# Kernel optimization log

Hardware: AMD Instinct MI355X
Metric: run time of the kernel (lower is better)

## Reference

```python
import jax, jax.numpy as jnp
import numpy as np

BATCH, PATH_DIM = 2048, 2048
SIG_DIM = 14  # 2 + 2^2 + 2^3, depth-3 signature of a 2-channel path


def setup_inputs() -> dict:
    key = jax.random.key(0)
    ks = jax.random.split(key, 6)
    x = jax.random.normal(ks[0], (BATCH, 1, PATH_DIM), jnp.float32)
    w1 = jax.random.normal(ks[1], (8, 1), jnp.float32) * 0.5   # Augment conv1 (kernel=1)
    b1 = jax.random.normal(ks[2], (8,), jnp.float32) * 0.1
    w2 = jax.random.normal(ks[3], (2, 8), jnp.float32) * 0.3   # Augment conv2 (kernel=1)
    b2 = jax.random.normal(ks[4], (2,), jnp.float32) * 0.1
    w_out = jax.random.normal(ks[5], (SIG_DIM,), jnp.float32) * 0.2  # Linear(14,1,bias=False)
    return dict(x=x, w1=w1, b1=b1, w2=w2, b2=b2, w_out=w_out)


def _forward(x, w1, b1, w2, b2, w_out):
    # Augment: pointwise MLP (Conv1d, kernel_size=1), channels 1 -> 8 -> 2, ReLU between.
    h = jax.nn.relu(jnp.einsum('bcl,hc->bhl', x, w1) + b1[None, :, None])
    path = jnp.einsum('bhl,oh->bol', h, w2) + b2[None, :, None]   # (B, 2, L)
    p = jnp.transpose(path, (0, 2, 1))                            # (B, L, 2)
    dx = p[:, 1:, :] - p[:, :-1, :]                               # (B, N=L-1, 2) increments

    # Depth-3 signature of each linear segment with increment v:
    #   level1 = v, level2 = v^{\otimes 2}/2, level3 = v^{\otimes 3}/6.
    s1 = dx
    s2 = 0.5 * jnp.einsum('bni,bnj->bnij', dx, dx)
    s3 = (1.0 / 6.0) * jnp.einsum('bni,bnj,bnk->bnijk', dx, dx, dx)

    def chen(carry, seg):
        # Chen's identity: signature of concatenated path = carry \otimes seg.
        a1, a2, a3 = carry
        g1, g2, g3 = seg
        c1 = a1 + g1
        c2 = a2 + jnp.einsum('bi,bj->bij', a1, g1) + g2
        c3 = (a3 + jnp.einsum('bij,bk->bijk', a2, g1)
              + jnp.einsum('bi,bjk->bijk', a1, g2) + g3)
        B = c1.shape[0]
        flat = jnp.concatenate([c1, c2.reshape(B, 4), c3.reshape(B, 8)], axis=-1)  # (B, 14)
        return (c1, c2, c3), flat

    B = dx.shape[0]
    dt = dx.dtype
    init = (jnp.zeros((B, 2), dt), jnp.zeros((B, 2, 2), dt), jnp.zeros((B, 2, 2, 2), dt))
    segs = (jnp.swapaxes(s1, 0, 1), jnp.swapaxes(s2, 0, 1), jnp.swapaxes(s3, 0, 1))
    _, sigs = jax.lax.scan(chen, init, segs)          # (N, B, 14): sig of each prefix x[:,:,:i+2]
    # Tiny output projection Linear(14 -> 1, no bias), then stack/transpose -> (B, N)
    return jnp.einsum('nbs,s->bn', sigs, w_out)


def reference(x, w1, b1, w2, b2, w_out):
    return _forward(x, w1, b1, w2, b2, w_out)
```

## Files before the change

### kernel.cpp

```cpp
#include <hip/hip_runtime.h>

#define LPTS  2048
#define NSEG  2047
#define TPB   256
#define STEPS 8
#define NBATCH 2048
#define NWAVE (TPB / 64)

template <int CTRL, int RMASK, bool BC>
__device__ __forceinline__ float dpp_f(float s) {
    return __int_as_float(__builtin_amdgcn_update_dpp(
        0, __float_as_int(s), CTRL, RMASK, 0xF, BC));
}


__device__ __forceinline__ void chen_step7(float s[7], float vx, float vy,
                                           const float WO[14], float WO78,
                                           float WO1112) {
    const float qxx = 0.5f * vx * vx;
    const float qxy = 0.5f * vx * vy;
    const float qyy = 0.5f * vy * vy;
    const float wx = fmaf(vx, (1.0f / 3.0f), s[0]);
    const float wy = fmaf(vy, (1.0f / 3.0f), s[1]);
    const float tvxx = fmaf(WO[7], vy, WO[6] * vx);
    const float tvxy = fmaf(WO[9], vy, WO[8] * vx);
    const float tvyx = fmaf(WO[11], vy, WO[10] * vx);
    const float tvyy = fmaf(WO[13], vy, WO[12] * vx);
    const float tqx = fmaf(WO[9], qyy, fmaf(WO78, qxy, WO[6] * qxx));
    const float tqy = fmaf(WO[13], qyy, fmaf(WO1112, qxy, WO[10] * qxx));
    float z1 = fmaf(s[2], tvxx, s[6]);
    z1 = fmaf(s[4], tvyx, z1);
    z1 = fmaf(wx, tqx, z1);
    float z2 = fmaf(s[5], tvyy, s[3] * tvxy);
    z2 = fmaf(wy, tqy, z2);
    s[6] = z1 + z2;
    const float ux = fmaf(vx, 0.5f, s[0]);
    const float uy = fmaf(vy, 0.5f, s[1]);
    s[2] = fmaf(ux, vx, s[2]);
    s[3] = fmaf(ux, vy, s[3]);
    s[4] = fmaf(uy, vx, s[4]);
    s[5] = fmaf(uy, vy, s[5]);
    s[0] += vx;
    s[1] += vy;
}

__device__ __forceinline__ void chen_combine7(const float a[7], float b[7],
                                              const float WO[14]) {
    const float tvxx = fmaf(WO[7], b[1], WO[6] * b[0]);
    const float tvxy = fmaf(WO[9], b[1], WO[8] * b[0]);
    const float tvyx = fmaf(WO[11], b[1], WO[10] * b[0]);
    const float tvyy = fmaf(WO[13], b[1], WO[12] * b[0]);
    const float ubx = fmaf(WO[9], b[5], fmaf(WO[8], b[4], fmaf(WO[7], b[3], WO[6] * b[2])));
    const float uby = fmaf(WO[13], b[5], fmaf(WO[12], b[4], fmaf(WO[11], b[3], WO[10] * b[2])));
    float z1 = fmaf(a[2], tvxx, a[6] + b[6]);
    z1 = fmaf(a[4], tvyx, z1);
    z1 = fmaf(a[0], ubx, z1);
    float z2 = fmaf(a[5], tvyy, a[3] * tvxy);
    z2 = fmaf(a[1], uby, z2);
    const float cxx = a[2] + fmaf(a[0], b[0], b[2]);
    const float cxy = a[3] + fmaf(a[0], b[1], b[3]);
    const float cyx = a[4] + fmaf(a[1], b[0], b[4]);
    const float cyy = a[5] + fmaf(a[1], b[1], b[5]);
    b[0] = a[0] + b[0];
    b[1] = a[1] + b[1];
    b[2] = cxx;
    b[3] = cxy;
    b[4] = cyx;
    b[5] = cyy;
    b[6] = z1 + z2;
}

__device__ __forceinline__ void augment(float x,
                                        const float W1[8], const float B1[8],
                                        const float W2x[8], const float W2y[8],
                                        float B2x, float B2y,
                                        float& px, float& py) {
    float ox = B2x, oy = B2y;
#pragma unroll
    for (int c = 0; c < 8; ++c) {
        float h = fmaxf(fmaf(W1[c], x, B1[c]), 0.0f);
        ox = fmaf(W2x[c], h, ox);
        oy = fmaf(W2y[c], h, oy);
    }
    px = ox;
    py = oy;
}

#define SCAN_ROUND(CTRL, RMASK, BC)                                     \
    {                                                                   \
        float p[7];                                                     \
        _Pragma("unroll")                                               \
        for (int i = 0; i < 7; ++i) p[i] = dpp_f<CTRL, RMASK, BC>(s[i]); \
        chen_combine7(p, s, WO);                                        \
    }

__global__ void sig_scan_kernel(
    const float* __restrict__ x, const float* __restrict__ w1,
    const float* __restrict__ b1, const float* __restrict__ w2,
    const float* __restrict__ b2, const float* __restrict__ wout,
    float* __restrict__ out) {
    __shared__ float wsum[NWAVE][8];

    const int t = threadIdx.x;
    const int lane = t & 63;
    const int wv = t >> 6;
    const int brow = blockIdx.x;
    const float* __restrict__ xrow = x + (size_t)brow * LPTS;

    float W1[8], B1[8], W2x[8], W2y[8];
#pragma unroll
    for (int c = 0; c < 8; ++c) {
        W1[c] = w1[c];
        B1[c] = b1[c];
        W2x[c] = w2[c];
        W2y[c] = w2[8 + c];
    }
    const float B2x = b2[0], B2y = b2[1];
    float WO[14];
#pragma unroll
    for (int i = 0; i < 14; ++i) WO[i] = wout[i];
    const float WO78 = WO[7] + WO[8];
    const float WO1112 = WO[11] + WO[12];

    const int n0 = t * STEPS;
    const float4 xa = *reinterpret_cast<const float4*>(xrow + n0);
    const float4 xb = *reinterpret_cast<const float4*>(xrow + n0 + 4);
    const int ib = (n0 + STEPS > LPTS - 1) ? (LPTS - 1) : (n0 + STEPS);
    const float x8 = xrow[ib];
    const float xv[STEPS + 1] = {xa.x, xa.y, xa.z, xa.w,
                                 xb.x, xb.y, xb.z, xb.w, x8};

    float vx[STEPS], vy[STEPS];
    float s[7] = {0, 0, 0, 0, 0, 0, 0};
    float ppx, ppy;
    augment(xv[0], W1, B1, W2x, W2y, B2x, B2y, ppx, ppy);
#pragma unroll
    for (int k = 0; k < STEPS; ++k) {
        float px, py;
        augment(xv[k + 1], W1, B1, W2x, W2y, B2x, B2y, px, py);
        vx[k] = px - ppx;
        vy[k] = py - ppy;
        ppx = px;
        ppy = py;
        chen_step7(s, vx[k], vy[k], WO, WO78, WO1112);
    }

    SCAN_ROUND(0x111, 0xF, true)
    SCAN_ROUND(0x112, 0xF, true)
    SCAN_ROUND(0x114, 0xF, true)
    SCAN_ROUND(0x118, 0xF, true)
    SCAN_ROUND(0x142, 0xA, false)
    SCAN_ROUND(0x143, 0xC, false)

    if (lane == 63) {
#pragma unroll
        for (int i = 0; i < 7; ++i) wsum[wv][i] = s[i];
    }
    __syncthreads();

    float a[7];
#pragma unroll
    for (int i = 0; i < 7; ++i) a[i] = dpp_f<0x138, 0xF, true>(s[i]);
    for (int w = wv - 1; w >= 0; --w) {
        float tw[7];
#pragma unroll
        for (int i = 0; i < 7; ++i) tw[i] = wsum[w][i];
        chen_combine7(tw, a, WO);
    }

    float* __restrict__ orow = out + (size_t)brow * NSEG;
#pragma unroll
    for (int k = 0; k < STEPS; ++k) {
        chen_step7(a, vx[k], vy[k], WO, WO78, WO1112);
        float o = a[6];
        o = fmaf(WO[0], a[0], o);
        o = fmaf(WO[1], a[1], o);
        o = fmaf(WO[2], a[2], o);
        o = fmaf(WO[3], a[3], o);
        o = fmaf(WO[4], a[4], o);
        o = fmaf(WO[5], a[5], o);
        const int n = n0 + k;
        if (n < NSEG) orow[n] = o;
    }
}

extern "C" void kernel_launch(void* const* d_in, const int* in_sizes, int n_in,
                              void* d_out, int out_size, void* d_ws, size_t ws_size,
                              hipStream_t stream) {
    const float* x  = (const float*)d_in[0];
    const float* w1 = (const float*)d_in[1];
    const float* b1 = (const float*)d_in[2];
    const float* w2 = (const float*)d_in[3];
    const float* b2 = (const float*)d_in[4];
    const float* wo = (const float*)d_in[5];
    float* out = (float*)d_out;
    sig_scan_kernel<<<NBATCH, TPB, 0, stream>>>(x, w1, b1, w2, b2, wo, out);
}
```

Before: 21.43 us.

## Process two rows per block and split per-thread chains into parallel halves

```diff
diff --git a/kernel.cpp b/kernel.cpp
--- a/kernel.cpp
+++ b/kernel.cpp
@@ -5,6 +5,8 @@
 #define TPB   256
 #define STEPS 8
 #define NBATCH 2048
+#define ROWS  2
+#define GRIDN (NBATCH / ROWS)
 #define NWAVE (TPB / 64)
 
 template <int CTRL, int RMASK, bool BC>
@@ -86,26 +88,24 @@
     py = oy;
 }
 
-#define SCAN_ROUND(CTRL, RMASK, BC)                                     \
-    {                                                                   \
-        float p[7];                                                     \
-        _Pragma("unroll")                                               \
+#define SCAN_ROUND(CTRL, RMASK, BC)                                      \
+    {                                                                    \
+        float p[7];                                                      \
+        _Pragma("unroll")                                                \
         for (int i = 0; i < 7; ++i) p[i] = dpp_f<CTRL, RMASK, BC>(s[i]); \
-        chen_combine7(p, s, WO);                                        \
-    }
-
-__global__ void sig_scan_kernel(
+        chen_combine7(p, s, WO);                                         \
+    }
+
+__global__ __launch_bounds__(TPB, 4) void sig_scan_kernel(
     const float* __restrict__ x, const float* __restrict__ w1,
     const float* __restrict__ b1, const float* __restrict__ w2,
     const float* __restrict__ b2, const float* __restrict__ wout,
     float* __restrict__ out) {
-    __shared__ float wsum[NWAVE][8];
+    __shared__ float wsum[2][NWAVE][8];
 
     const int t = threadIdx.x;
     const int lane = t & 63;
     const int wv = t >> 6;
-    const int brow = blockIdx.x;
-    const float* __restrict__ xrow = x + (size_t)brow * LPTS;
 
     float W1[8], B1[8], W2x[8], W2y[8];
 #pragma unroll
@@ -122,65 +122,97 @@
     const float WO78 = WO[7] + WO[8];
     const float WO1112 = WO[11] + WO[12];
 
-    const int n0 = t * STEPS;
-    const float4 xa = *reinterpret_cast<const float4*>(xrow + n0);
-    const float4 xb = *reinterpret_cast<const float4*>(xrow + n0 + 4);
-    const int ib = (n0 + STEPS > LPTS - 1) ? (LPTS - 1) : (n0 + STEPS);
-    const float x8 = xrow[ib];
-    const float xv[STEPS + 1] = {xa.x, xa.y, xa.z, xa.w,
-                                 xb.x, xb.y, xb.z, xb.w, x8};
-
-    float vx[STEPS], vy[STEPS];
-    float s[7] = {0, 0, 0, 0, 0, 0, 0};
-    float ppx, ppy;
-    augment(xv[0], W1, B1, W2x, W2y, B2x, B2y, ppx, ppy);
-#pragma unroll
-    for (int k = 0; k < STEPS; ++k) {
-        float px, py;
-        augment(xv[k + 1], W1, B1, W2x, W2y, B2x, B2y, px, py);
-        vx[k] = px - ppx;
-        vy[k] = py - ppy;
-        ppx = px;
-        ppy = py;
-        chen_step7(s, vx[k], vy[k], WO, WO78, WO1112);
-    }
-
-    SCAN_ROUND(0x111, 0xF, true)
-    SCAN_ROUND(0x112, 0xF, true)
-    SCAN_ROUND(0x114, 0xF, true)
-    SCAN_ROUND(0x118, 0xF, true)
-    SCAN_ROUND(0x142, 0xA, false)
-    SCAN_ROUND(0x143, 0xC, false)
-
-    if (lane == 63) {
-#pragma unroll
-        for (int i = 0; i < 7; ++i) wsum[wv][i] = s[i];
-    }
-    __syncthreads();
-
-    float a[7];
-#pragma unroll
-    for (int i = 0; i < 7; ++i) a[i] = dpp_f<0x138, 0xF, true>(s[i]);
-    for (int w = wv - 1; w >= 0; --w) {
-        float tw[7];
-#pragma unroll
-        for (int i = 0; i < 7; ++i) tw[i] = wsum[w][i];
-        chen_combine7(tw, a, WO);
-    }
-
-    float* __restrict__ orow = out + (size_t)brow * NSEG;
-#pragma unroll
-    for (int k = 0; k < STEPS; ++k) {
-        chen_step7(a, vx[k], vy[k], WO, WO78, WO1112);
-        float o = a[6];
-        o = fmaf(WO[0], a[0], o);
-        o = fmaf(WO[1], a[1], o);
-        o = fmaf(WO[2], a[2], o);
-        o = fmaf(WO[3], a[3], o);
-        o = fmaf(WO[4], a[4], o);
-        o = fmaf(WO[5], a[5], o);
-        const int n = n0 + k;
-        if (n < NSEG) orow[n] = o;
+    for (int r = 0; r < ROWS; ++r) {
+        const int brow = blockIdx.x + r * GRIDN;
+        const float* __restrict__ xrow = x + (size_t)brow * LPTS;
+
+        const int n0 = t * STEPS;
+        const float4 xa = *reinterpret_cast<const float4*>(xrow + n0);
+        const float4 xb = *reinterpret_cast<const float4*>(xrow + n0 + 4);
+        const int ib = (n0 + STEPS > LPTS - 1) ? (LPTS - 1) : (n0 + STEPS);
+        const float x8 = xrow[ib];
+        const float xv[STEPS + 1] = {xa.x, xa.y, xa.z, xa.w,
+                                     xb.x, xb.y, xb.z, xb.w, x8};
+
+        float vx[STEPS], vy[STEPS];
+        {
+            float ppx, ppy;
+            augment(xv[0], W1, B1, W2x, W2y, B2x, B2y, ppx, ppy);
+#pragma unroll
+            for (int k = 0; k < STEPS; ++k) {
+                float px, py;
+                augment(xv[k + 1], W1, B1, W2x, W2y, B2x, B2y, px, py);
+                vx[k] = px - ppx;
+                vy[k] = py - ppy;
+                ppx = px;
+                ppy = py;
+            }
+        }
+        float s_lo[7] = {0, 0, 0, 0, 0, 0, 0};
+        float s[7] = {0, 0, 0, 0, 0, 0, 0};
+#pragma unroll
+        for (int k = 0; k < 4; ++k) {
+            chen_step7(s_lo, vx[k], vy[k], WO, WO78, WO1112);
+            chen_step7(s, vx[k + 4], vy[k + 4], WO, WO78, WO1112);
+        }
+        chen_combine7(s_lo, s, WO);
+
+        SCAN_ROUND(0x111, 0xF, true)
+        SCAN_ROUND(0x112, 0xF, true)
+        SCAN_ROUND(0x114, 0xF, true)
+        SCAN_ROUND(0x118, 0xF, true)
+        SCAN_ROUND(0x142, 0xA, false)
+        SCAN_ROUND(0x143, 0xC, false)
+
+        if (lane == 63) {
+#pragma unroll
+            for (int i = 0; i < 7; ++i) wsum[r & 1][wv][i] = s[i];
+        }
+        __syncthreads();
+
+        float a[7];
+#pragma unroll
+        for (int i = 0; i < 7; ++i) a[i] = dpp_f<0x138, 0xF, true>(s[i]);
+        for (int w = wv - 1; w >= 0; --w) {
+            float tw[7];
+#pragma unroll
+            for (int i = 0; i < 7; ++i) tw[i] = wsum[r & 1][w][i];
+            chen_combine7(tw, a, WO);
+        }
+
+        float a_hi[7];
+#pragma unroll
+        for (int i = 0; i < 7; ++i) a_hi[i] = s_lo[i];
+        chen_combine7(a, a_hi, WO);
+
+        float* __restrict__ orow = out + (size_t)brow * NSEG;
+        float og[STEPS];
+#pragma unroll
+        for (int k = 0; k < 4; ++k) {
+            chen_step7(a, vx[k], vy[k], WO, WO78, WO1112);
+            float o = a[6];
+            o = fmaf(WO[0], a[0], o);
+            o = fmaf(WO[1], a[1], o);
+            o = fmaf(WO[2], a[2], o);
+            o = fmaf(WO[3], a[3], o);
+            o = fmaf(WO[4], a[4], o);
+            o = fmaf(WO[5], a[5], o);
+            og[k] = o;
+            chen_step7(a_hi, vx[k + 4], vy[k + 4], WO, WO78, WO1112);
+            float o2 = a_hi[6];
+            o2 = fmaf(WO[0], a_hi[0], o2);
+            o2 = fmaf(WO[1], a_hi[1], o2);
+            o2 = fmaf(WO[2], a_hi[2], o2);
+            o2 = fmaf(WO[3], a_hi[3], o2);
+            o2 = fmaf(WO[4], a_hi[4], o2);
+            o2 = fmaf(WO[5], a_hi[5], o2);
+            og[k + 4] = o2;
+        }
+#pragma unroll
+        for (int k = 0; k < STEPS; ++k) {
+            const int n = n0 + k;
+            if (n < NSEG) orow[n] = og[k];
+        }
     }
 }
 
@@ -194,5 +226,5 @@
     const float* b2 = (const float*)d_in[4];
     const float* wo = (const float*)d_in[5];
     float* out = (float*)d_out;
-    sig_scan_kernel<<<NBATCH, TPB, 0, stream>>>(x, w1, b1, w2, b2, wo, out);
-}
+    sig_scan_kernel<<<GRIDN, TPB, 0, stream>>>(x, w1, b1, w2, b2, wo, out);
+}
```

Result: slower. 24.21 us (+13.0%).

## Split wave scan into level-1/2 prefix scan plus additive scalar level-3 scan

Applied to the files above, without the earlier changes.

```diff
diff --git a/kernel.cpp b/kernel.cpp
--- a/kernel.cpp
+++ b/kernel.cpp
@@ -70,6 +70,19 @@
     b[6] = z1 + z2;
 }
 
+__device__ __forceinline__ void chen_combine6(const float a[6], float b[6]) {
+    const float cxx = a[2] + fmaf(a[0], b[0], b[2]);
+    const float cxy = a[3] + fmaf(a[0], b[1], b[3]);
+    const float cyx = a[4] + fmaf(a[1], b[0], b[4]);
+    const float cyy = a[5] + fmaf(a[1], b[1], b[5]);
+    b[0] = a[0] + b[0];
+    b[1] = a[1] + b[1];
+    b[2] = cxx;
+    b[3] = cxy;
+    b[4] = cyx;
+    b[5] = cyy;
+}
+
 __device__ __forceinline__ void augment(float x,
                                         const float W1[8], const float B1[8],
                                         const float W2x[8], const float W2y[8],
@@ -86,13 +99,15 @@
     py = oy;
 }
 
-#define SCAN_ROUND(CTRL, RMASK, BC)                                     \
-    {                                                                   \
-        float p[7];                                                     \
-        _Pragma("unroll")                                               \
-        for (int i = 0; i < 7; ++i) p[i] = dpp_f<CTRL, RMASK, BC>(s[i]); \
-        chen_combine7(p, s, WO);                                        \
-    }
+#define SCAN6_ROUND(CTRL, RMASK, BC)                                     \
+    {                                                                    \
+        float p[6];                                                      \
+        _Pragma("unroll")                                                \
+        for (int i = 0; i < 6; ++i) p[i] = dpp_f<CTRL, RMASK, BC>(s[i]); \
+        chen_combine6(p, s);                                             \
+    }
+
+#define USCAN_ROUND(CTRL, RMASK, BC) u += dpp_f<CTRL, RMASK, BC>(u);
 
 __global__ void sig_scan_kernel(
     const float* __restrict__ x, const float* __restrict__ w1,
@@ -145,22 +160,55 @@
         chen_step7(s, vx[k], vy[k], WO, WO78, WO1112);
     }
 
-    SCAN_ROUND(0x111, 0xF, true)
-    SCAN_ROUND(0x112, 0xF, true)
-    SCAN_ROUND(0x114, 0xF, true)
-    SCAN_ROUND(0x118, 0xF, true)
-    SCAN_ROUND(0x142, 0xA, false)
-    SCAN_ROUND(0x143, 0xC, false)
+    float sl[7];
+#pragma unroll
+    for (int i = 0; i < 7; ++i) sl[i] = s[i];
+
+    SCAN6_ROUND(0x111, 0xF, true)
+    SCAN6_ROUND(0x112, 0xF, true)
+    SCAN6_ROUND(0x114, 0xF, true)
+    SCAN6_ROUND(0x118, 0xF, true)
+    SCAN6_ROUND(0x142, 0xA, false)
+    SCAN6_ROUND(0x143, 0xC, false)
+
+    float e[6];
+#pragma unroll
+    for (int i = 0; i < 6; ++i) e[i] = dpp_f<0x138, 0xF, true>(s[i]);
+
+    float u;
+    {
+        const float tvxx = fmaf(WO[7], sl[1], WO[6] * sl[0]);
+        const float tvxy = fmaf(WO[9], sl[1], WO[8] * sl[0]);
+        const float tvyx = fmaf(WO[11], sl[1], WO[10] * sl[0]);
+        const float tvyy = fmaf(WO[13], sl[1], WO[12] * sl[0]);
+        const float ubx = fmaf(WO[9], sl[5], fmaf(WO[8], sl[4], fmaf(WO[7], sl[3], WO[6] * sl[2])));
+        const float uby = fmaf(WO[13], sl[5], fmaf(WO[12], sl[4], fmaf(WO[11], sl[3], WO[10] * sl[2])));
+        u = fmaf(e[2], tvxx, sl[6]);
+        u = fmaf(e[3], tvxy, u);
+        u = fmaf(e[4], tvyx, u);
+        u = fmaf(e[5], tvyy, u);
+        u = fmaf(e[0], ubx, u);
+        u = fmaf(e[1], uby, u);
+    }
+
+    USCAN_ROUND(0x111, 0xF, true)
+    USCAN_ROUND(0x112, 0xF, true)
+    USCAN_ROUND(0x114, 0xF, true)
+    USCAN_ROUND(0x118, 0xF, true)
+    USCAN_ROUND(0x142, 0xA, false)
+    USCAN_ROUND(0x143, 0xC, false)
 
     if (lane == 63) {
 #pragma unroll
-        for (int i = 0; i < 7; ++i) wsum[wv][i] = s[i];
+        for (int i = 0; i < 6; ++i) wsum[wv][i] = s[i];
+        wsum[wv][6] = u;
     }
     __syncthreads();
 
     float a[7];
 #pragma unroll
-    for (int i = 0; i < 7; ++i) a[i] = dpp_f<0x138, 0xF, true>(s[i]);
+    for (int i = 0; i < 6; ++i) a[i] = e[i];
+    a[6] = dpp_f<0x138, 0xF, true>(u);
     for (int w = wv - 1; w >= 0; --w) {
         float tw[7];
 #pragma unroll
```

Result: faster. 19.73 us (-7.9%).
